# Performance work log

Measured on AMD Instinct MI355X. Metric: run time of the kernel, lower is better.

## Reference

```python
import jax, jax.numpy as jnp
import numpy as np
import math

B, S, HID = 2, 2048, 512
HEADS = 8
DH = HID // HEADS  # 64


def _euler_alpha(seq_len, dh):
    # alpha[t, i] = t * 10000^(-2i/dh), shape [S, dh//2]
    pos = jnp.arange(seq_len, dtype=jnp.float32)[:, None]
    ids = jnp.arange(dh // 2, dtype=jnp.float32)
    freq = jnp.power(10000.0, -2.0 * ids / dh)
    return pos * freq  # [S, dh//2]


def euler_rotate(x, delta):
    # x: [B, H, S, DH] -> polar rotation (EulerFormer, type='ro', no bias b)
    r = x[..., ::2]
    p = x[..., 1::2]
    lam = jnp.sqrt(r * r + p * p)
    theta = jnp.arctan2(p, r) * delta + _euler_alpha(x.shape[2], x.shape[3])[None, None]
    r2 = lam * jnp.cos(theta)
    p2 = lam * jnp.sin(theta)
    # interleave back: stack last dim then reshape
    out = jnp.stack([r2, p2], axis=-1)
    return out.reshape(x.shape)


def setup_inputs() -> dict:
    key = jax.random.key(0)
    ks = jax.random.split(key, 12)
    sc = 1.0 / math.sqrt(HID)
    return {
        "q": jax.random.normal(ks[0], (B, S, HID), jnp.float32),
        "k": jax.random.normal(ks[1], (B, S, HID), jnp.float32),
        "v": jax.random.normal(ks[2], (B, S, HID), jnp.float32),
        "Wq": jax.random.normal(ks[3], (HID, HID), jnp.float32) * sc,
        "bq": jnp.zeros((HID,), jnp.float32),
        "Wk": jax.random.normal(ks[4], (HID, HID), jnp.float32) * sc,
        "bk": jnp.zeros((HID,), jnp.float32),
        "Wv": jax.random.normal(ks[5], (HID, HID), jnp.float32) * sc,
        "bv": jnp.zeros((HID,), jnp.float32),
        "Wo": jax.random.normal(ks[6], (HID, HID), jnp.float32) * sc,
        "bo": jnp.zeros((HID,), jnp.float32),
        "delta_q": jnp.ones((1,), jnp.float32),
        "delta_k": jnp.ones((1,), jnp.float32),
    }


def reference(q, k, v, Wq, bq, Wk, bk, Wv, bv, Wo, bo, delta_q, delta_k):
    b = q.shape[0]
    def proj(x, W, bias):
        y = x @ W.T + bias  # torch Linear: x W^T + b
        return y.reshape(b, -1, HEADS, DH).transpose(0, 2, 1, 3)  # [B,H,S,DH]
    qh = proj(q, Wq, bq)
    kh = proj(k, Wk, bk)
    vh = proj(v, Wv, bv)
    qh = euler_rotate(qh, delta_q)
    kh = euler_rotate(kh, delta_k)
    corr = jnp.einsum('bhqd,bhkd->bhqk', qh, kh) / math.sqrt(DH)
    s = corr.shape[-1]
    causal = jnp.triu(jnp.full((s, s), -jnp.inf, jnp.float32), k=1)
    corr = corr + causal[None, None]
    attn = jax.nn.softmax(corr, axis=-1)
    hidden = jnp.einsum('bhqk,bhkd->bhqd', attn, vh)
    hidden = hidden.transpose(0, 2, 1, 3).reshape(b, -1, HID)
    return hidden @ Wo.T + bo
```

## Files before the change

kernel.cpp:

```cpp
#include <hip/hip_runtime.h>
#include <math.h>

constexpr int B_   = 2;
constexpr int S_   = 2048;
constexpr int HID_ = 512;
constexpr int H_   = 8;
constexpr int DH_  = 64;
constexpr int M_   = B_ * S_;

typedef unsigned short ushort_t;
typedef unsigned int   uint_t;
typedef __attribute__((ext_vector_type(4))) float  f32x4;
typedef __attribute__((ext_vector_type(8))) __bf16 bf16x8;
typedef __attribute__((ext_vector_type(4))) uint_t u32x4;

#define MFMA16(A, Bv, C) __builtin_amdgcn_mfma_f32_16x16x32_bf16( \
    __builtin_bit_cast(bf16x8, (A)), __builtin_bit_cast(bf16x8, (Bv)), (C), 0, 0, 0)

__device__ __forceinline__ uint2 splitPair(float x0, float x1) {
    uint_t b0 = __float_as_uint(x0), b1 = __float_as_uint(x1);
    uint_t hi = (b0 >> 16) | (b1 & 0xFFFF0000u);
    float h0 = __uint_as_float(b0 & 0xFFFF0000u);
    float h1 = __uint_as_float(b1 & 0xFFFF0000u);
    uint_t l0 = __float_as_uint(x0 - h0), l1 = __float_as_uint(x1 - h1);
    uint_t lo = (l0 >> 16) | (l1 & 0xFFFF0000u);
    return make_uint2(hi, lo);
}

__device__ __forceinline__ void splitOne(float x, ushort_t& hi, ushort_t& lo) {
    uint_t b = __float_as_uint(x);
    hi = (ushort_t)(b >> 16);
    float h = __uint_as_float(b & 0xFFFF0000u);
    lo = (ushort_t)(__float_as_uint(x - h) >> 16);
}

template <int MODE>
__device__ __forceinline__ void gemm_mfma_body(const float* __restrict__ A,
                                               const float* __restrict__ W,
                                               const float* __restrict__ bias,
                                               ushort_t* __restrict__ outHi,
                                               ushort_t* __restrict__ outLo,
                                               float* __restrict__ outF,
                                               const float* __restrict__ delta)
{
    constexpr int K_ = HID_;
    __shared__ __align__(16) ushort_t Ah[64][40], Al[64][40];
    __shared__ __align__(16) ushort_t Bh[64][40], Bl[64][40];

    const int t    = threadIdx.x;
    const int lane = t & 63;
    const int wid  = t >> 6;
    const int wr   = wid >> 1;
    const int wc   = wid & 1;
    const int a    = lane & 15;
    const int g    = lane >> 4;
    const int bm   = blockIdx.x * 64;
    const int bn   = blockIdx.y * 64;

    const int srow = t >> 2, sg8 = t & 3;
    const float* Ap = A + (size_t)(bm + srow) * K_ + sg8 * 8;
    const float* Wp = W + (size_t)(bn + srow) * K_ + sg8 * 8;

    float4 ra0 = *(const float4*)Ap,       ra1 = *(const float4*)(Ap + 4);
    float4 rb0 = *(const float4*)Wp,       rb1 = *(const float4*)(Wp + 4);

    f32x4 acc[2][2];
#pragma unroll
    for (int mt = 0; mt < 2; ++mt)
#pragma unroll
        for (int nt = 0; nt < 2; ++nt)
#pragma unroll
            for (int r = 0; r < 4; ++r) acc[mt][nt][r] = 0.f;

    for (int k0 = 0; k0 < K_; k0 += 32) {
        __syncthreads();
        {
            const uint2 s0 = splitPair(ra0.x, ra0.y), s1 = splitPair(ra0.z, ra0.w);
            const uint2 s2 = splitPair(ra1.x, ra1.y), s3 = splitPair(ra1.z, ra1.w);
            *(u32x4*)&Ah[srow][sg8 * 8] = u32x4{s0.x, s1.x, s2.x, s3.x};
            *(u32x4*)&Al[srow][sg8 * 8] = u32x4{s0.y, s1.y, s2.y, s3.y};
            const uint2 t0 = splitPair(rb0.x, rb0.y), t1 = splitPair(rb0.z, rb0.w);
            const uint2 t2 = splitPair(rb1.x, rb1.y), t3 = splitPair(rb1.z, rb1.w);
            *(u32x4*)&Bh[srow][sg8 * 8] = u32x4{t0.x, t1.x, t2.x, t3.x};
            *(u32x4*)&Bl[srow][sg8 * 8] = u32x4{t0.y, t1.y, t2.y, t3.y};
        }
        if (k0 + 32 < K_) {
            const float* pa = Ap + k0 + 32;
            const float* pw = Wp + k0 + 32;
            ra0 = *(const float4*)pa; ra1 = *(const float4*)(pa + 4);
            rb0 = *(const float4*)pw; rb1 = *(const float4*)(pw + 4);
        }
        __syncthreads();

        u32x4 afh[2], afl[2], bfh[2], bfl[2];
#pragma unroll
        for (int mt = 0; mt < 2; ++mt) {
            const int ar = wr * 32 + mt * 16 + a;
            afh[mt] = *(const u32x4*)&Ah[ar][g * 8];
            afl[mt] = *(const u32x4*)&Al[ar][g * 8];
        }
#pragma unroll
        for (int nt = 0; nt < 2; ++nt) {
            const int br = wc * 32 + nt * 16 + a;
            bfh[nt] = *(const u32x4*)&Bh[br][g * 8];
            bfl[nt] = *(const u32x4*)&Bl[br][g * 8];
        }
#pragma unroll
        for (int nt = 0; nt < 2; ++nt)
#pragma unroll
            for (int mt = 0; mt < 2; ++mt) {
                acc[mt][nt] = MFMA16(afh[mt], bfh[nt], acc[mt][nt]);
                acc[mt][nt] = MFMA16(afh[mt], bfl[nt], acc[mt][nt]);
                acc[mt][nt] = MFMA16(afl[mt], bfh[nt], acc[mt][nt]);
            }
    }

    const float del = (MODE == 1 || MODE == 2) ? delta[0] : 0.f;
#pragma unroll
    for (int mt = 0; mt < 2; ++mt) {
#pragma unroll
        for (int nt = 0; nt < 2; ++nt) {
            const int n  = bn + wc * 32 + nt * 16 + a;
            const float bb = bias[n];
            f32x4 vals;
#pragma unroll
            for (int r = 0; r < 4; ++r) vals[r] = acc[mt][nt][r] + bb;

            if (MODE == 0) {
#pragma unroll
                for (int r = 0; r < 4; ++r) {
                    const int m = bm + wr * 32 + mt * 16 + g * 4 + r;
                    outF[(size_t)m * HID_ + n] = vals[r];
                }
            } else if (MODE == 1 || MODE == 2) {
                const int d  = n & 63;
                const int h  = n >> 6;
                const float freq = exp2f(-(float)(d >> 1) * 0.4152410118609203f);
#pragma unroll
                for (int r = 0; r < 4; ++r) {
                    const int m = bm + wr * 32 + mt * 16 + g * 4 + r;
                    const int b = m >> 11, s = m & (S_ - 1);
                    const float val  = vals[r];
                    const float part = __shfl_xor(val, 1);
                    const float rr = (a & 1) ? part : val;
                    const float pp = (a & 1) ? val  : part;
                    const float lam = sqrtf(rr * rr + pp * pp);
                    const float th  = atan2f(pp, rr) * del + (float)s * freq;
                    float sn, cs;
                    sincosf(th, &sn, &cs);
                    float o = (a & 1) ? lam * sn : lam * cs;
                    if (MODE == 1) o *= 0.125f;
                    ushort_t hi, lo;
                    splitOne(o, hi, lo);
                    const size_t idx = (((size_t)b * H_ + h) * S_ + s) * DH_ + d;
                    outHi[idx] = hi;
                    outLo[idx] = lo;
                }
            } else {
                const int d  = n & 63;
                const int h  = n >> 6;
                const int m0 = bm + wr * 32 + mt * 16 + g * 4;
                const int b  = m0 >> 11, s0 = m0 & (S_ - 1);
                const uint2 p01 = splitPair(vals[0], vals[1]);
                const uint2 p23 = splitPair(vals[2], vals[3]);
                const size_t idx = (((size_t)b * H_ + h) * DH_ + d) * S_ + s0;
                *(uint2*)&outHi[idx] = make_uint2(p01.x, p23.x);
                *(uint2*)&outLo[idx] = make_uint2(p01.y, p23.y);
            }
        }
    }
}

struct QkvPtrs {
    const float* A[3];
    const float* W[3];
    const float* bias[3];
    ushort_t*    hi[3];
    ushort_t*    lo[3];
    const float* del[2];
};

__global__ __launch_bounds__(256)
void gemm_qkv_kernel(QkvPtrs p)
{
    const int z = blockIdx.z;
    if (z == 0)      gemm_mfma_body<1>(p.A[0], p.W[0], p.bias[0], p.hi[0], p.lo[0], nullptr, p.del[0]);
    else if (z == 1) gemm_mfma_body<2>(p.A[1], p.W[1], p.bias[1], p.hi[1], p.lo[1], nullptr, p.del[1]);
    else             gemm_mfma_body<3>(p.A[2], p.W[2], p.bias[2], p.hi[2], p.lo[2], nullptr, nullptr);
}

__global__ __launch_bounds__(256)
void gemm_out_kernel(const float* __restrict__ A, const float* __restrict__ W,
                     const float* __restrict__ bias, float* __restrict__ out)
{
    gemm_mfma_body<0>(A, W, bias, nullptr, nullptr, out, nullptr);
}

__global__ __launch_bounds__(256)
void attn_mfma_kernel(const ushort_t* __restrict__ qhi_g, const ushort_t* __restrict__ qlo_g,
                      const ushort_t* __restrict__ khi_g, const ushort_t* __restrict__ klo_g,
                      const ushort_t* __restrict__ vhi_g, const ushort_t* __restrict__ vlo_g,
                      float* __restrict__ hidden)
{
    __shared__ __align__(16) ushort_t Khi[64][72];
    __shared__ __align__(16) ushort_t Klo[64][72];
    __shared__ __align__(16) ushort_t Vhi[64][72];
    __shared__ __align__(16) ushort_t Vlo[64][72];
    __shared__ __align__(16) ushort_t Ph[4][16][72];
    __shared__ __align__(16) ushort_t Pl[4][16][72];

    const int t    = threadIdx.x;
    const int lane = t & 63;
    const int wid  = t >> 6;
    const int a    = lane & 15;
    const int g    = lane >> 4;
    const int qt   = 31 - blockIdx.x;
    const int bh   = blockIdx.y;

    u32x4 qhi[2], qlo[2];
    {
        const size_t qrow = ((size_t)bh * S_ + (size_t)qt * 64 + wid * 16 + a) * DH_;
#pragma unroll
        for (int kit = 0; kit < 2; ++kit) {
            qhi[kit] = *(const u32x4*)&qhi_g[qrow + kit * 32 + g * 8];
            qlo[kit] = *(const u32x4*)&qlo_g[qrow + kit * 32 + g * 8];
        }
    }

    f32x4 Oacc[4];
#pragma unroll
    for (int nt = 0; nt < 4; ++nt)
#pragma unroll
        for (int r = 0; r < 4; ++r) Oacc[nt][r] = 0.f;
    float mrow[4] = {-INFINITY, -INFINITY, -INFINITY, -INFINITY};
    float lrow[4] = {0.f, 0.f, 0.f, 0.f};

    for (int kt = 0; kt <= qt; ++kt) {
        const ushort_t* Ksh = khi_g + ((size_t)bh * S_ + kt * 64) * DH_;
        const ushort_t* Ksl = klo_g + ((size_t)bh * S_ + kt * 64) * DH_;
        const ushort_t* Vsh = vhi_g + (size_t)bh * DH_ * S_ + kt * 64;
        const ushort_t* Vsl = vlo_g + (size_t)bh * DH_ * S_ + kt * 64;
        __syncthreads();
#pragma unroll
        for (int i = 0; i < 2; ++i) {
            const int seg = t + i * 256;
            const int row = seg >> 3, c8 = (seg & 7) * 8;
            *(u32x4*)&Khi[row][c8] = *(const u32x4*)&Ksh[row * 64 + c8];
            *(u32x4*)&Klo[row][c8] = *(const u32x4*)&Ksl[row * 64 + c8];
            *(u32x4*)&Vhi[row][c8] = *(const u32x4*)&Vsh[(size_t)row * S_ + c8];
            *(u32x4*)&Vlo[row][c8] = *(const u32x4*)&Vsl[(size_t)row * S_ + c8];
        }
        __syncthreads();

        f32x4 Sacc[4];
#pragma unroll
        for (int nt = 0; nt < 4; ++nt)
#pragma unroll
            for (int r = 0; r < 4; ++r) Sacc[nt][r] = 0.f;
#pragma unroll
        for (int kit = 0; kit < 2; ++kit) {
#pragma unroll
            for (int nt = 0; nt < 4; ++nt) {
                const u32x4 kbh = *(const u32x4*)&Khi[a + 16 * nt][kit * 32 + g * 8];
                const u32x4 kbl = *(const u32x4*)&Klo[a + 16 * nt][kit * 32 + g * 8];
                Sacc[nt] = MFMA16(qhi[kit], kbh, Sacc[nt]);
                Sacc[nt] = MFMA16(qhi[kit], kbl, Sacc[nt]);
                Sacc[nt] = MFMA16(qlo[kit], kbh, Sacc[nt]);
            }
        }

        float sc[4][4];
        const int q0 = qt * 64 + wid * 16 + g * 4;
        const int k0 = kt * 64 + a;
#pragma unroll
        for (int nt = 0; nt < 4; ++nt)
#pragma unroll
            for (int r = 0; r < 4; ++r)
                sc[nt][r] = (k0 + 16 * nt <= q0 + r) ? Sacc[nt][r] : -INFINITY;

#pragma unroll
        for (int r = 0; r < 4; ++r) {
            float mr = fmaxf(fmaxf(sc[0][r], sc[1][r]), fmaxf(sc[2][r], sc[3][r]));
            mr = fmaxf(mr, __shfl_xor(mr, 1));
            mr = fmaxf(mr, __shfl_xor(mr, 2));
            mr = fmaxf(mr, __shfl_xor(mr, 4));
            mr = fmaxf(mr, __shfl_xor(mr, 8));
            const float mnew = fmaxf(mrow[r], mr);
            const float fac  = __expf(mrow[r] - mnew);
            mrow[r] = mnew;
            float ps = 0.f;
            const int q = g * 4 + r;
#pragma unroll
            for (int nt = 0; nt < 4; ++nt) {
                const float p = __expf(sc[nt][r] - mnew);
                ps += p;
                ushort_t phi, plo;
                splitOne(p, phi, plo);
                Ph[wid][q][a + 16 * nt] = phi;
                Pl[wid][q][a + 16 * nt] = plo;
            }
            lrow[r] = lrow[r] * fac + ps;
#pragma unroll
            for (int nt = 0; nt < 4; ++nt) Oacc[nt][r] *= fac;
        }

#pragma unroll
        for (int kit = 0; kit < 2; ++kit) {
            const u32x4 pah = *(const u32x4*)&Ph[wid][a][kit * 32 + g * 8];
            const u32x4 pal = *(const u32x4*)&Pl[wid][a][kit * 32 + g * 8];
#pragma unroll
            for (int nt = 0; nt < 4; ++nt) {
                const u32x4 vbh = *(const u32x4*)&Vhi[a + 16 * nt][kit * 32 + g * 8];
                const u32x4 vbl = *(const u32x4*)&Vlo[a + 16 * nt][kit * 32 + g * 8];
                Oacc[nt] = MFMA16(pah, vbh, Oacc[nt]);
                Oacc[nt] = MFMA16(pah, vbl, Oacc[nt]);
                Oacc[nt] = MFMA16(pal, vbh, Oacc[nt]);
            }
        }
    }

    float inv[4];
#pragma unroll
    for (int r = 0; r < 4; ++r) {
        float ls = lrow[r];
        ls += __shfl_xor(ls, 1);
        ls += __shfl_xor(ls, 2);
        ls += __shfl_xor(ls, 4);
        ls += __shfl_xor(ls, 8);
        inv[r] = 1.f / ls;
    }
    const int b = bh >> 3, h = bh & 7;
#pragma unroll
    for (int r = 0; r < 4; ++r) {
        const int qg = qt * 64 + wid * 16 + g * 4 + r;
        float* dst = hidden + ((size_t)b * S_ + qg) * HID_ + h * DH_ + a;
#pragma unroll
        for (int nt = 0; nt < 4; ++nt) dst[16 * nt] = Oacc[nt][r] * inv[r];
    }
}

extern "C" void kernel_launch(void* const* d_in, const int* in_sizes, int n_in,
                              void* d_out, int out_size, void* d_ws, size_t ws_size,
                              hipStream_t stream)
{
    const float* q  = (const float*)d_in[0];
    const float* k  = (const float*)d_in[1];
    const float* v  = (const float*)d_in[2];
    const float* Wq = (const float*)d_in[3];
    const float* bq = (const float*)d_in[4];
    const float* Wk = (const float*)d_in[5];
    const float* bk = (const float*)d_in[6];
    const float* Wv = (const float*)d_in[7];
    const float* bv = (const float*)d_in[8];
    const float* Wo = (const float*)d_in[9];
    const float* bo = (const float*)d_in[10];
    const float* dq = (const float*)d_in[11];
    const float* dk = (const float*)d_in[12];
    float* out = (float*)d_out;

    const size_t TEN = (size_t)B_ * S_ * HID_;
    ushort_t* qhi = (ushort_t*)d_ws;
    ushort_t* qlo = qhi + TEN;
    ushort_t* khi = qlo + TEN;
    ushort_t* klo = khi + TEN;
    ushort_t* vhi = klo + TEN;
    ushort_t* vlo = vhi + TEN;
    float* hidden = (float*)(vlo + TEN);

    QkvPtrs p;
    p.A[0] = q; p.W[0] = Wq; p.bias[0] = bq; p.hi[0] = qhi; p.lo[0] = qlo;
    p.A[1] = k; p.W[1] = Wk; p.bias[1] = bk; p.hi[1] = khi; p.lo[1] = klo;
    p.A[2] = v; p.W[2] = Wv; p.bias[2] = bv; p.hi[2] = vhi; p.lo[2] = vlo;
    p.del[0] = dq; p.del[1] = dk;

    gemm_qkv_kernel<<<dim3(M_ / 64, HID_ / 64, 3), 256, 0, stream>>>(p);
    attn_mfma_kernel<<<dim3(S_ / 64, B_ * H_), 256, 0, stream>>>(qhi, qlo, khi, klo, vhi, vlo, hidden);
    gemm_out_kernel<<<dim3(M_ / 64, HID_ / 64), 256, 0, stream>>>(hidden, Wo, bo, out);
}
```

Before: 243.0 us.

## Enlarge GEMM M-tile to 128 and register-prefetch next K/V tile in attention

```diff
diff --git a/kernel.cpp b/kernel.cpp
--- a/kernel.cpp
+++ b/kernel.cpp
@@ -44,8 +44,8 @@
                                                const float* __restrict__ delta)
 {
     constexpr int K_ = HID_;
-    __shared__ __align__(16) ushort_t Ah[64][40], Al[64][40];
-    __shared__ __align__(16) ushort_t Bh[64][40], Bl[64][40];
+    __shared__ __align__(16) ushort_t Ah[128][40], Al[128][40];
+    __shared__ __align__(16) ushort_t Bh[64][40],  Bl[64][40];
 
     const int t    = threadIdx.x;
     const int lane = t & 63;
@@ -54,19 +54,21 @@
     const int wc   = wid & 1;
     const int a    = lane & 15;
     const int g    = lane >> 4;
-    const int bm   = blockIdx.x * 64;
+    const int bm   = blockIdx.x * 128;
     const int bn   = blockIdx.y * 64;
 
-    const int srow = t >> 2, sg8 = t & 3;
-    const float* Ap = A + (size_t)(bm + srow) * K_ + sg8 * 8;
-    const float* Wp = W + (size_t)(bn + srow) * K_ + sg8 * 8;
-
-    float4 ra0 = *(const float4*)Ap,       ra1 = *(const float4*)(Ap + 4);
-    float4 rb0 = *(const float4*)Wp,       rb1 = *(const float4*)(Wp + 4);
-
-    f32x4 acc[2][2];
-#pragma unroll
-    for (int mt = 0; mt < 2; ++mt)
+    const int arow = t >> 1, acol = (t & 1) * 16;
+    const int wrow = t >> 2, wcol = (t & 3) * 8;
+    const float* Ap = A + (size_t)(bm + arow) * K_ + acol;
+    const float* Wp = W + (size_t)(bn + wrow) * K_ + wcol;
+
+    float4 ra0 = ((const float4*)Ap)[0], ra1 = ((const float4*)Ap)[1];
+    float4 ra2 = ((const float4*)Ap)[2], ra3 = ((const float4*)Ap)[3];
+    float4 rw0 = ((const float4*)Wp)[0], rw1 = ((const float4*)Wp)[1];
+
+    f32x4 acc[4][2];
+#pragma unroll
+    for (int mt = 0; mt < 4; ++mt)
 #pragma unroll
         for (int nt = 0; nt < 2; ++nt)
 #pragma unroll
@@ -77,25 +79,30 @@
         {
             const uint2 s0 = splitPair(ra0.x, ra0.y), s1 = splitPair(ra0.z, ra0.w);
             const uint2 s2 = splitPair(ra1.x, ra1.y), s3 = splitPair(ra1.z, ra1.w);
-            *(u32x4*)&Ah[srow][sg8 * 8] = u32x4{s0.x, s1.x, s2.x, s3.x};
-            *(u32x4*)&Al[srow][sg8 * 8] = u32x4{s0.y, s1.y, s2.y, s3.y};
-            const uint2 t0 = splitPair(rb0.x, rb0.y), t1 = splitPair(rb0.z, rb0.w);
-            const uint2 t2 = splitPair(rb1.x, rb1.y), t3 = splitPair(rb1.z, rb1.w);
-            *(u32x4*)&Bh[srow][sg8 * 8] = u32x4{t0.x, t1.x, t2.x, t3.x};
-            *(u32x4*)&Bl[srow][sg8 * 8] = u32x4{t0.y, t1.y, t2.y, t3.y};
+            *(u32x4*)&Ah[arow][acol] = u32x4{s0.x, s1.x, s2.x, s3.x};
+            *(u32x4*)&Al[arow][acol] = u32x4{s0.y, s1.y, s2.y, s3.y};
+            const uint2 s4 = splitPair(ra2.x, ra2.y), s5 = splitPair(ra2.z, ra2.w);
+            const uint2 s6 = splitPair(ra3.x, ra3.y), s7 = splitPair(ra3.z, ra3.w);
+            *(u32x4*)&Ah[arow][acol + 8] = u32x4{s4.x, s5.x, s6.x, s7.x};
+            *(u32x4*)&Al[arow][acol + 8] = u32x4{s4.y, s5.y, s6.y, s7.y};
+            const uint2 t0 = splitPair(rw0.x, rw0.y), t1 = splitPair(rw0.z, rw0.w);
+            const uint2 t2 = splitPair(rw1.x, rw1.y), t3 = splitPair(rw1.z, rw1.w);
+            *(u32x4*)&Bh[wrow][wcol] = u32x4{t0.x, t1.x, t2.x, t3.x};
+            *(u32x4*)&Bl[wrow][wcol] = u32x4{t0.y, t1.y, t2.y, t3.y};
         }
         if (k0 + 32 < K_) {
             const float* pa = Ap + k0 + 32;
             const float* pw = Wp + k0 + 32;
-            ra0 = *(const float4*)pa; ra1 = *(const float4*)(pa + 4);
-            rb0 = *(const float4*)pw; rb1 = *(const float4*)(pw + 4);
+            ra0 = ((const float4*)pa)[0]; ra1 = ((const float4*)pa)[1];
+            ra2 = ((const float4*)pa)[2]; ra3 = ((const float4*)pa)[3];
+            rw0 = ((const float4*)pw)[0]; rw1 = ((const float4*)pw)[1];
         }
         __syncthreads();
 
-        u32x4 afh[2], afl[2], bfh[2], bfl[2];
-#pragma unroll
-        for (int mt = 0; mt < 2; ++mt) {
-            const int ar = wr * 32 + mt * 16 + a;
+        u32x4 afh[4], afl[4], bfh[2], bfl[2];
+#pragma unroll
+        for (int mt = 0; mt < 4; ++mt) {
+            const int ar = wr * 64 + mt * 16 + a;
             afh[mt] = *(const u32x4*)&Ah[ar][g * 8];
             afl[mt] = *(const u32x4*)&Al[ar][g * 8];
         }
@@ -108,7 +115,7 @@
 #pragma unroll
         for (int nt = 0; nt < 2; ++nt)
 #pragma unroll
-            for (int mt = 0; mt < 2; ++mt) {
+            for (int mt = 0; mt < 4; ++mt) {
                 acc[mt][nt] = MFMA16(afh[mt], bfh[nt], acc[mt][nt]);
                 acc[mt][nt] = MFMA16(afh[mt], bfl[nt], acc[mt][nt]);
                 acc[mt][nt] = MFMA16(afl[mt], bfh[nt], acc[mt][nt]);
@@ -117,7 +124,7 @@
 
     const float del = (MODE == 1 || MODE == 2) ? delta[0] : 0.f;
 #pragma unroll
-    for (int mt = 0; mt < 2; ++mt) {
+    for (int mt = 0; mt < 4; ++mt) {
 #pragma unroll
         for (int nt = 0; nt < 2; ++nt) {
             const int n  = bn + wc * 32 + nt * 16 + a;
@@ -129,7 +136,7 @@
             if (MODE == 0) {
 #pragma unroll
                 for (int r = 0; r < 4; ++r) {
-                    const int m = bm + wr * 32 + mt * 16 + g * 4 + r;
+                    const int m = bm + wr * 64 + mt * 16 + g * 4 + r;
                     outF[(size_t)m * HID_ + n] = vals[r];
                 }
             } else if (MODE == 1 || MODE == 2) {
@@ -138,7 +145,7 @@
                 const float freq = exp2f(-(float)(d >> 1) * 0.4152410118609203f);
 #pragma unroll
                 for (int r = 0; r < 4; ++r) {
-                    const int m = bm + wr * 32 + mt * 16 + g * 4 + r;
+                    const int m = bm + wr * 64 + mt * 16 + g * 4 + r;
                     const int b = m >> 11, s = m & (S_ - 1);
                     const float val  = vals[r];
                     const float part = __shfl_xor(val, 1);
@@ -159,7 +166,7 @@
             } else {
                 const int d  = n & 63;
                 const int h  = n >> 6;
-                const int m0 = bm + wr * 32 + mt * 16 + g * 4;
+                const int m0 = bm + wr * 64 + mt * 16 + g * 4;
                 const int b  = m0 >> 11, s0 = m0 & (S_ - 1);
                 const uint2 p01 = splitPair(vals[0], vals[1]);
                 const uint2 p23 = splitPair(vals[2], vals[3]);
@@ -227,6 +234,29 @@
         }
     }
 
+    const ushort_t* Kbh = khi_g + (size_t)bh * S_ * DH_;
+    const ushort_t* Kbl = klo_g + (size_t)bh * S_ * DH_;
+    const ushort_t* Vbh = vhi_g + (size_t)bh * DH_ * S_;
+    const ushort_t* Vbl = vlo_g + (size_t)bh * DH_ * S_;
+
+    const int r0 = t >> 3,          c0 = (t & 7) * 8;
+    const int r1 = (t + 256) >> 3,  c1 = ((t + 256) & 7) * 8;
+
+    u32x4 rKh[2], rKl[2], rVh[2], rVl[2];
+    auto loadKV = [&](int kt) {
+        const size_t ko = (size_t)kt * 64 * DH_;
+        const size_t vo = (size_t)kt * 64;
+        rKh[0] = *(const u32x4*)&Kbh[ko + r0 * 64 + c0];
+        rKh[1] = *(const u32x4*)&Kbh[ko + r1 * 64 + c1];
+        rKl[0] = *(const u32x4*)&Kbl[ko + r0 * 64 + c0];
+        rKl[1] = *(const u32x4*)&Kbl[ko + r1 * 64 + c1];
+        rVh[0] = *(const u32x4*)&Vbh[vo + (size_t)r0 * S_ + c0];
+        rVh[1] = *(const u32x4*)&Vbh[vo + (size_t)r1 * S_ + c1];
+        rVl[0] = *(const u32x4*)&Vbl[vo + (size_t)r0 * S_ + c0];
+        rVl[1] = *(const u32x4*)&Vbl[vo + (size_t)r1 * S_ + c1];
+    };
+    loadKV(0);
+
     f32x4 Oacc[4];
 #pragma unroll
     for (int nt = 0; nt < 4; ++nt)
@@ -236,20 +266,12 @@
     float lrow[4] = {0.f, 0.f, 0.f, 0.f};
 
     for (int kt = 0; kt <= qt; ++kt) {
-        const ushort_t* Ksh = khi_g + ((size_t)bh * S_ + kt * 64) * DH_;
-        const ushort_t* Ksl = klo_g + ((size_t)bh * S_ + kt * 64) * DH_;
-        const ushort_t* Vsh = vhi_g + (size_t)bh * DH_ * S_ + kt * 64;
-        const ushort_t* Vsl = vlo_g + (size_t)bh * DH_ * S_ + kt * 64;
         __syncthreads();
-#pragma unroll
-        for (int i = 0; i < 2; ++i) {
-            const int seg = t + i * 256;
-            const int row = seg >> 3, c8 = (seg & 7) * 8;
-            *(u32x4*)&Khi[row][c8] = *(const u32x4*)&Ksh[row * 64 + c8];
-            *(u32x4*)&Klo[row][c8] = *(const u32x4*)&Ksl[row * 64 + c8];
-            *(u32x4*)&Vhi[row][c8] = *(const u32x4*)&Vsh[(size_t)row * S_ + c8];
-            *(u32x4*)&Vlo[row][c8] = *(const u32x4*)&Vsl[(size_t)row * S_ + c8];
-        }
+        *(u32x4*)&Khi[r0][c0] = rKh[0];  *(u32x4*)&Khi[r1][c1] = rKh[1];
+        *(u32x4*)&Klo[r0][c0] = rKl[0];  *(u32x4*)&Klo[r1][c1] = rKl[1];
+        *(u32x4*)&Vhi[r0][c0] = rVh[0];  *(u32x4*)&Vhi[r1][c1] = rVh[1];
+        *(u32x4*)&Vlo[r0][c0] = rVl[0];  *(u32x4*)&Vlo[r1][c1] = rVl[1];
+        if (kt < qt) loadKV(kt + 1);
         __syncthreads();
 
         f32x4 Sacc[4];
@@ -373,7 +395,7 @@
     p.A[2] = v; p.W[2] = Wv; p.bias[2] = bv; p.hi[2] = vhi; p.lo[2] = vlo;
     p.del[0] = dq; p.del[1] = dk;
 
-    gemm_qkv_kernel<<<dim3(M_ / 64, HID_ / 64, 3), 256, 0, stream>>>(p);
+    gemm_qkv_kernel<<<dim3(M_ / 128, HID_ / 64, 3), 256, 0, stream>>>(p);
     attn_mfma_kernel<<<dim3(S_ / 64, B_ * H_), 256, 0, stream>>>(qhi, qlo, khi, klo, vhi, vlo, hidden);
-    gemm_out_kernel<<<dim3(M_ / 64, HID_ / 64), 256, 0, stream>>>(hidden, Wo, bo, out);
-}
+    gemm_out_kernel<<<dim3(M_ / 128, HID_ / 64), 256, 0, stream>>>(hidden, Wo, bo, out);
+}
```

New measurement: 279.3 us. 1.15x slower.
